# Kernel optimization log

Hardware: AMD Instinct MI355X
Metric: run time of the kernel (lower is better)

Reference implementation:

```python
import jax, jax.numpy as jnp
import numpy as np

TOKENS_PER_SCALE = [1, 4, 16, 64, 256]  # CLS + 2x2,4x4,8x8,16x16 patch scales = 341
TOTAL = sum(TOKENS_PER_SCALE)
NUM_HEADS = 12


def build_scale_causal_mask():
    # 0 where allowed, -inf where blocked. CLS row (scale 0) attends everywhere;
    # tokens in scale i may attend to scales j <= i (and always to CLS).
    cum = np.cumsum([0] + TOKENS_PER_SCALE)
    m = np.zeros((TOTAL, TOTAL), dtype=np.float32)
    for i in range(1, len(TOKENS_PER_SCALE)):
        for j in range(len(TOKENS_PER_SCALE)):
            if j > i:
                m[cum[i]:cum[i + 1], cum[j]:cum[j + 1]] = -np.inf
    return jnp.asarray(m)


def setup_inputs() -> dict:
    key = jax.random.key(0)
    k1, k2, k3, k4, k5 = jax.random.split(key, 5)
    B, N, D = 64, TOTAL, 768
    x = jax.random.normal(k1, (B, N, D), dtype=jnp.float32)
    qkv_w = jax.random.normal(k2, (3 * D, D), dtype=jnp.float32) * 0.02
    qkv_b = jax.random.normal(k3, (3 * D,), dtype=jnp.float32) * 0.02
    proj_w = jax.random.normal(k4, (D, D), dtype=jnp.float32) * 0.02
    proj_b = jax.random.normal(k5, (D,), dtype=jnp.float32) * 0.02
    return {"x": x, "qkv_w": qkv_w, "qkv_b": qkv_b, "proj_w": proj_w, "proj_b": proj_b}


def reference(x, qkv_w, qkv_b, proj_w, proj_b):
    B, N, D = x.shape
    H = NUM_HEADS
    hd = D // H
    scale = hd ** -0.5
    mask = build_scale_causal_mask()  # [N, N]

    qkv = jnp.einsum('bnd,ed->bne', x, qkv_w) + qkv_b  # [B, N, 3D]
    qkv = qkv.reshape(B, N, 3, H, hd)
    q = jnp.transpose(qkv[:, :, 0], (0, 2, 1, 3))  # [B, H, N, hd]
    k = jnp.transpose(qkv[:, :, 1], (0, 2, 1, 3))
    v = jnp.transpose(qkv[:, :, 2], (0, 2, 1, 3))

    attn = jnp.einsum('bhqd,bhkd->bhqk', q, k) * scale + mask  # [B, H, N, N]
    attn = jax.nn.softmax(attn, axis=-1)
    out = jnp.einsum('bhqk,bhkd->bhqd', attn, v)  # [B, H, N, hd]
    out = jnp.transpose(out, (0, 2, 1, 3)).reshape(B, N, D)
    out = jnp.einsum('bnd,ed->bne', out, proj_w) + proj_b
    return out
```

## Files before the change

kernel.cpp:

```cpp
#include <hip/hip_runtime.h>
#include <hip/hip_bf16.h>

typedef float  f32x4  __attribute__((ext_vector_type(4)));
typedef __bf16 bf16x4 __attribute__((ext_vector_type(4)));
typedef __bf16 bf16x8 __attribute__((ext_vector_type(8)));

#define B_SZ  64
#define NTOK  341
#define DM    768
#define NH    12
#define HD    64
#define MTOT  (B_SZ*NTOK)
#define MP    21888
#define EQKV  2304

#define EXP2F(x) __builtin_amdgcn_exp2f(x)

__device__ __forceinline__ void gload_lds16(const __bf16* g, void* l) {
    __builtin_amdgcn_global_load_lds(
        (const __attribute__((address_space(1))) void*)g,
        (__attribute__((address_space(3))) void*)l, 16, 0, 0);
}

__global__ void cvt_kernel(const float* __restrict__ in, __bf16* __restrict__ out, int n4) {
    int i = blockIdx.x * blockDim.x + threadIdx.x;
    const int stride = gridDim.x * blockDim.x;
    for (; i < n4; i += stride) {
        const float4 f = ((const float4*)in)[i];
        bf16x4 v;
        v[0] = (__bf16)f.x; v[1] = (__bf16)f.y; v[2] = (__bf16)f.z; v[3] = (__bf16)f.w;
        ((bf16x4*)out)[i] = v;
    }
}

template <int EPI, int EN, int NT>
__global__ __launch_bounds__(256) void gemm128(
    const __bf16* __restrict__ A, const __bf16* __restrict__ Bw,
    const float* __restrict__ bias,
    __bf16* __restrict__ obf, float* __restrict__ of32)
{
    __shared__ __bf16 As[2][128 * 64];
    __shared__ __bf16 Bs[2][128 * 64];

    const int tid  = threadIdx.x;
    const int lane = tid & 63;
    const int w    = tid >> 6;
    const int wm   = w >> 1, wn = w & 1;
    const int qi   = lane & 15;
    const int g    = lane >> 4;

    const int nwg = gridDim.x;
    const int bid = blockIdx.x;
    const int qq = nwg >> 3, rr = nwg & 7;
    const int xcd = bid & 7, idx = bid >> 3;
    const int wg = (xcd < rr ? xcd * (qq + 1) : rr * (qq + 1) + (xcd - rr) * qq) + idx;
    const int mtile = wg / NT;
    const int ntile = wg % NT;
    const long a_row0 = (long)mtile * 128;
    const long n0     = (long)ntile * 128;

    const int slot = lane & 7;
    const __bf16* aP[4];
    const __bf16* bP[4];
#pragma unroll
    for (int it = 0; it < 4; ++it) {
        const int lrow = it * 32 + w * 8 + (lane >> 3);
        const int scol = (slot ^ (lrow & 7)) * 8;
        aP[it] = A + (a_row0 + lrow) * DM + scol;
        const int gcol = (lrow & 64) | ((lrow & 15) << 2) | ((lrow >> 4) & 3);
        bP[it] = Bw + (n0 + gcol) * DM + scol;
    }

    const f32x4 fzero = {0.f, 0.f, 0.f, 0.f};
    f32x4 acc[4][4];
#pragma unroll
    for (int i = 0; i < 4; ++i)
#pragma unroll
        for (int j = 0; j < 4; ++j) acc[i][j] = fzero;

#define STAGE(P, K0) do { \
    _Pragma("unroll") for (int it = 0; it < 4; ++it) { \
        gload_lds16(aP[it] + (K0), (char*)(&As[P][0]) + it * 4096 + w * 1024); \
        gload_lds16(bP[it] + (K0), (char*)(&Bs[P][0]) + it * 4096 + w * 1024); \
    } } while (0)

    STAGE(0, 0);
    __syncthreads();

    int cur = 0;
    for (int k0 = 0; k0 < DM; k0 += 64) {
        if (k0 + 64 < DM) STAGE(cur ^ 1, k0 + 64);

        const __bf16* pA = &As[cur][0];
        const __bf16* pB = &Bs[cur][0];
        bf16x8 af[4][2], bfr[4][2];
#pragma unroll
        for (int i = 0; i < 4; ++i) {
            const int fr = wm * 64 + i * 16 + qi;
#pragma unroll
            for (int ks = 0; ks < 2; ++ks)
                af[i][ks] = *(const bf16x8*)(pA + fr * 64 + (((ks << 2) + g) ^ (fr & 7)) * 8);
        }
#pragma unroll
        for (int j = 0; j < 4; ++j) {
            const int frb = wn * 64 + j * 16 + qi;
#pragma unroll
            for (int ks = 0; ks < 2; ++ks)
                bfr[j][ks] = *(const bf16x8*)(pB + frb * 64 + (((ks << 2) + g) ^ (frb & 7)) * 8);
        }
#pragma unroll
        for (int ks = 0; ks < 2; ++ks)
#pragma unroll
            for (int j = 0; j < 4; ++j)
#pragma unroll
                for (int i = 0; i < 4; ++i)
                    acc[i][j] = __builtin_amdgcn_mfma_f32_16x16x32_bf16(
                        af[i][ks], bfr[j][ks], acc[i][j], 0, 0, 0);

        __syncthreads();
        cur ^= 1;
    }
#undef STAGE

    const long ge0 = n0 + wn * 64 + qi * 4;
    const float4 b4 = *(const float4*)(bias + ge0);
    const float mul = (EPI == 0 && (n0 + wn * 64) < DM) ? 0.125f * 1.44269504f : 1.f;
#pragma unroll
    for (int i = 0; i < 4; ++i) {
#pragma unroll
        for (int r = 0; r < 4; ++r) {
            const long m = a_row0 + wm * 64 + i * 16 + g * 4 + r;
            if (m < MTOT) {
                if (EPI == 0) {
                    bf16x4 pv;
                    pv[0] = (__bf16)((acc[i][0][r] + b4.x) * mul);
                    pv[1] = (__bf16)((acc[i][1][r] + b4.y) * mul);
                    pv[2] = (__bf16)((acc[i][2][r] + b4.z) * mul);
                    pv[3] = (__bf16)((acc[i][3][r] + b4.w) * mul);
                    *(bf16x4*)(obf + m * EN + ge0) = pv;
                } else {
                    float4 o;
                    o.x = acc[i][0][r] + b4.x;
                    o.y = acc[i][1][r] + b4.y;
                    o.z = acc[i][2][r] + b4.z;
                    o.w = acc[i][3][r] + b4.w;
                    *(float4*)(of32 + m * EN + ge0) = o;
                }
            }
        }
    }
}

template <int NJ>
__device__ __forceinline__ void attn_group(
    const __bf16* __restrict__ qkv, const char* vL, __bf16* __restrict__ ao,
    long rowb, int h, int q0, int qi, int g)
{
    int qrow = q0 + qi; if (qrow > NTOK - 1) qrow = NTOK - 1;
    const __bf16* qsrc = qkv + (rowb + qrow) * EQKV + h * HD + g * 8;
    const bf16x8 qf0 = *(const bf16x8*)(qsrc);
    const bf16x8 qf1 = *(const bf16x8*)(qsrc + 32);

    const int qg = q0 + qi;
    int limit;
    if (qg == 0)       limit = NTOK;
    else if (qg < 5)   limit = 5;
    else if (qg < 21)  limit = 21;
    else if (qg < 85)  limit = 85;
    else               limit = NTOK;

    const f32x4 fzero = {0.f, 0.f, 0.f, 0.f};
    f32x4 oacc[4] = {fzero, fzero, fzero, fzero};
    float sum = 0.f;

    const __bf16* kbase = qkv + rowb * EQKV + DM + h * HD + g * 8;
    const int xd = (qi & 7) ^ ((qi >> 3) & 7);

#pragma unroll 2
    for (int j = 0; j < NJ; ++j) {
        const int kr0 = 32 * j + qi;
        int kr1 = kr0 + 16; if (kr1 > NTOK - 1) kr1 = NTOK - 1;
        const __bf16* k0p = kbase + (long)kr0 * EQKV;
        const __bf16* k1p = kbase + (long)kr1 * EQKV;
        const bf16x8 k00 = *(const bf16x8*)(k0p);
        const bf16x8 k01 = *(const bf16x8*)(k0p + 32);
        const bf16x8 k10 = *(const bf16x8*)(k1p);
        const bf16x8 k11 = *(const bf16x8*)(k1p + 32);

        f32x4 s0 = __builtin_amdgcn_mfma_f32_16x16x32_bf16(k00, qf0, fzero, 0, 0, 0);
        s0 = __builtin_amdgcn_mfma_f32_16x16x32_bf16(k01, qf1, s0, 0, 0, 0);
        f32x4 s1 = __builtin_amdgcn_mfma_f32_16x16x32_bf16(k10, qf0, fzero, 0, 0, 0);
        s1 = __builtin_amdgcn_mfma_f32_16x16x32_bf16(k11, qf1, s1, 0, 0, 0);

        bf16x8 pf;
#pragma unroll
        for (int r = 0; r < 4; ++r) {
            const int k0i = 32 * j + g * 4 + r;
            const float p0 = (k0i < limit) ? EXP2F(s0[r]) : 0.f;
            sum += p0; pf[r] = (__bf16)p0;
            const int k1i = k0i + 16;
            const float p1 = (k1i < limit) ? EXP2F(s1[r]) : 0.f;
            sum += p1; pf[4 + r] = (__bf16)p1;
        }

#pragma unroll
        for (int db = 0; db < 4; ++db) {
            const int d  = db * 16 + qi;
            const int sp = (4 * j + g) ^ xd ^ ((2 * db) & 7);
            const bf16x8 vf = *(const bf16x8*)(vL + d * 768 + sp * 16);
            oacc[db] = __builtin_amdgcn_mfma_f32_16x16x32_bf16(vf, pf, oacc[db], 0, 0, 0);
        }
    }

    sum += __shfl_xor(sum, 16);
    sum += __shfl_xor(sum, 32);
    const float rinv = 1.f / sum;

    if (qg < NTOK) {
        const long orow = (rowb + qg) * DM + h * HD;
#pragma unroll
        for (int db = 0; db < 4; ++db) {
            bf16x4 pv;
#pragma unroll
            for (int r = 0; r < 4; ++r) pv[r] = (__bf16)(oacc[db][r] * rinv);
            *(bf16x4*)(ao + orow + db * 16 + g * 4) = pv;
        }
    }
}

__global__ __launch_bounds__(512) void attn_kernel(
    const __bf16* __restrict__ qkv, __bf16* __restrict__ ao)
{
    const int h = blockIdx.x;
    const int b = blockIdx.y;
    const long rowb = (long)b * NTOK;

    __shared__ char vL[64 * 768];

    const int tid  = threadIdx.x;
    const int lane = tid & 63;
    const int w    = tid >> 6;

#pragma unroll
    for (int it = 0; it < 6; ++it) {
        const int c = it * 512 + tid;
        if (c < 2816) {
            const int n  = c >> 3;
            const int dc = (c & 7) << 3;
            bf16x8 e;
            if (n < NTOK) e = *(const bf16x8*)(qkv + (rowb + n) * EQKV + 1536 + h * HD + dc);
            else { e[0]=e[1]=e[2]=e[3]=e[4]=e[5]=e[6]=e[7] = (__bf16)0.f; }
            const int s   = ((n >> 5) << 2) | ((n >> 2) & 3);
            const int off = (((n >> 4) & 1) << 3) | ((n & 3) << 1);
            const int x   = c & 7;
#pragma unroll
            for (int i = 0; i < 8; ++i) {
                const int sp = s ^ i ^ x;
                *(__bf16*)(vL + (dc + i) * 768 + sp * 16 + off) = e[i];
            }
        }
    }
    __syncthreads();

    const int g  = lane >> 4;
    const int qi = lane & 15;

    for (int gi = w; gi < 22; gi += 8) {
        const int q0 = gi * 16;
        if (gi >= 1 && gi <= 4)
            attn_group<3>(qkv, vL, ao, rowb, h, q0, qi, g);
        else
            attn_group<11>(qkv, vL, ao, rowb, h, q0, qi, g);
    }
}

extern "C" void kernel_launch(void* const* d_in, const int* in_sizes, int n_in,
                              void* d_out, int out_size, void* d_ws, size_t ws_size,
                              hipStream_t stream) {
    const float* x      = (const float*)d_in[0];
    const float* qkv_w  = (const float*)d_in[1];
    const float* qkv_b  = (const float*)d_in[2];
    const float* proj_w = (const float*)d_in[3];
    const float* proj_b = (const float*)d_in[4];
    float* out = (float*)d_out;

    char* ws = (char*)d_ws;
    constexpr size_t XB_BYTES  = (size_t)MP * DM * 2;
    constexpr size_t WQ_OFF    = XB_BYTES;
    constexpr size_t WP_OFF    = WQ_OFF + (size_t)EQKV * DM * 2;
    constexpr size_t QKV_OFF   = WP_OFF + (size_t)DM * DM * 2;

    __bf16* xb  = (__bf16*)(ws);
    __bf16* wq  = (__bf16*)(ws + WQ_OFF);
    __bf16* wp  = (__bf16*)(ws + WP_OFF);
    __bf16* qkv = (__bf16*)(ws + QKV_OFF);

    cvt_kernel<<<2048, 256, 0, stream>>>(x,      xb, MTOT * DM / 4);
    cvt_kernel<<<1728, 256, 0, stream>>>(qkv_w,  wq, EQKV * DM / 4);
    cvt_kernel<<<576,  256, 0, stream>>>(proj_w, wp, DM * DM / 4);

    gemm128<0, EQKV, 18><<<171 * 18, 256, 0, stream>>>(xb, wq, qkv_b, qkv, nullptr);
    attn_kernel<<<dim3(NH, B_SZ), 512, 0, stream>>>(qkv, xb);
    gemm128<1, DM, 6><<<171 * 6, 256, 0, stream>>>(xb, wp, proj_b, nullptr, out);
}
```

Measured before the change: 267.4 us.

## Process three query groups per wave to share K loads and V fragments

The attention kernel's per-wave loop over query groups is replaced by one pass in which each wave holds three 16-row query tiles at once. Each K fragment loaded from global memory and each V fragment read from LDS now feeds MFMAs for all three tiles, which cuts redundant loads and gives the scheduler more independent MFMA work. In exchange, the short three-iteration path for the early scales is dropped, so every tile runs all 11 key blocks. Two waves also compute out-of-range padding tiles whose results are thrown away, and accumulator register use triples.

```diff
diff --git a/kernel.cpp b/kernel.cpp
--- a/kernel.cpp
+++ b/kernel.cpp
@@ -151,83 +151,6 @@
     }
 }
 
-template <int NJ>
-__device__ __forceinline__ void attn_group(
-    const __bf16* __restrict__ qkv, const char* vL, __bf16* __restrict__ ao,
-    long rowb, int h, int q0, int qi, int g)
-{
-    int qrow = q0 + qi; if (qrow > NTOK - 1) qrow = NTOK - 1;
-    const __bf16* qsrc = qkv + (rowb + qrow) * EQKV + h * HD + g * 8;
-    const bf16x8 qf0 = *(const bf16x8*)(qsrc);
-    const bf16x8 qf1 = *(const bf16x8*)(qsrc + 32);
-
-    const int qg = q0 + qi;
-    int limit;
-    if (qg == 0)       limit = NTOK;
-    else if (qg < 5)   limit = 5;
-    else if (qg < 21)  limit = 21;
-    else if (qg < 85)  limit = 85;
-    else               limit = NTOK;
-
-    const f32x4 fzero = {0.f, 0.f, 0.f, 0.f};
-    f32x4 oacc[4] = {fzero, fzero, fzero, fzero};
-    float sum = 0.f;
-
-    const __bf16* kbase = qkv + rowb * EQKV + DM + h * HD + g * 8;
-    const int xd = (qi & 7) ^ ((qi >> 3) & 7);
-
-#pragma unroll 2
-    for (int j = 0; j < NJ; ++j) {
-        const int kr0 = 32 * j + qi;
-        int kr1 = kr0 + 16; if (kr1 > NTOK - 1) kr1 = NTOK - 1;
-        const __bf16* k0p = kbase + (long)kr0 * EQKV;
-        const __bf16* k1p = kbase + (long)kr1 * EQKV;
-        const bf16x8 k00 = *(const bf16x8*)(k0p);
-        const bf16x8 k01 = *(const bf16x8*)(k0p + 32);
-        const bf16x8 k10 = *(const bf16x8*)(k1p);
-        const bf16x8 k11 = *(const bf16x8*)(k1p + 32);
-
-        f32x4 s0 = __builtin_amdgcn_mfma_f32_16x16x32_bf16(k00, qf0, fzero, 0, 0, 0);
-        s0 = __builtin_amdgcn_mfma_f32_16x16x32_bf16(k01, qf1, s0, 0, 0, 0);
-        f32x4 s1 = __builtin_amdgcn_mfma_f32_16x16x32_bf16(k10, qf0, fzero, 0, 0, 0);
-        s1 = __builtin_amdgcn_mfma_f32_16x16x32_bf16(k11, qf1, s1, 0, 0, 0);
-
-        bf16x8 pf;
-#pragma unroll
-        for (int r = 0; r < 4; ++r) {
-            const int k0i = 32 * j + g * 4 + r;
-            const float p0 = (k0i < limit) ? EXP2F(s0[r]) : 0.f;
-            sum += p0; pf[r] = (__bf16)p0;
-            const int k1i = k0i + 16;
-            const float p1 = (k1i < limit) ? EXP2F(s1[r]) : 0.f;
-            sum += p1; pf[4 + r] = (__bf16)p1;
-        }
-
-#pragma unroll
-        for (int db = 0; db < 4; ++db) {
-            const int d  = db * 16 + qi;
-            const int sp = (4 * j + g) ^ xd ^ ((2 * db) & 7);
-            const bf16x8 vf = *(const bf16x8*)(vL + d * 768 + sp * 16);
-            oacc[db] = __builtin_amdgcn_mfma_f32_16x16x32_bf16(vf, pf, oacc[db], 0, 0, 0);
-        }
-    }
-
-    sum += __shfl_xor(sum, 16);
-    sum += __shfl_xor(sum, 32);
-    const float rinv = 1.f / sum;
-
-    if (qg < NTOK) {
-        const long orow = (rowb + qg) * DM + h * HD;
-#pragma unroll
-        for (int db = 0; db < 4; ++db) {
-            bf16x4 pv;
-#pragma unroll
-            for (int r = 0; r < 4; ++r) pv[r] = (__bf16)(oacc[db][r] * rinv);
-            *(bf16x4*)(ao + orow + db * 16 + g * 4) = pv;
-        }
-    }
-}
-
 __global__ __launch_bounds__(512) void attn_kernel(
     const __bf16* __restrict__ qkv, __bf16* __restrict__ ao)
 {
@@ -265,12 +188,87 @@
     const int g  = lane >> 4;
     const int qi = lane & 15;
 
-    for (int gi = w; gi < 22; gi += 8) {
-        const int q0 = gi * 16;
-        if (gi >= 1 && gi <= 4)
-            attn_group<3>(qkv, vL, ao, rowb, h, q0, qi, g);
-        else
-            attn_group<11>(qkv, vL, ao, rowb, h, q0, qi, g);
+    bf16x8 qf0[3], qf1[3];
+    int   qg[3], limit[3];
+#pragma unroll
+    for (int s = 0; s < 3; ++s) {
+        const int gi = w + 8 * s;
+        const int q  = gi * 16 + qi;
+        qg[s] = q;
+        const int qrow = (q > NTOK - 1) ? (NTOK - 1) : q;
+        const __bf16* qsrc = qkv + (rowb + qrow) * EQKV + h * HD + g * 8;
+        qf0[s] = *(const bf16x8*)(qsrc);
+        qf1[s] = *(const bf16x8*)(qsrc + 32);
+        limit[s] = (q == 0) ? NTOK : (q < 5 ? 5 : (q < 21 ? 21 : (q < 85 ? 85 : NTOK)));
+    }
+
+    const f32x4 fzero = {0.f, 0.f, 0.f, 0.f};
+    f32x4 oacc[3][4];
+    float sum[3] = {0.f, 0.f, 0.f};
+#pragma unroll
+    for (int s = 0; s < 3; ++s)
+#pragma unroll
+        for (int db = 0; db < 4; ++db) oacc[s][db] = fzero;
+
+    const __bf16* kbase = qkv + rowb * EQKV + DM + h * HD + g * 8;
+    const int xd = (qi & 7) ^ ((qi >> 3) & 7);
+
+    for (int j = 0; j < 11; ++j) {
+        const int kr0 = 32 * j + qi;
+        int kr1 = kr0 + 16; if (kr1 > NTOK - 1) kr1 = NTOK - 1;
+        const __bf16* k0p = kbase + (long)kr0 * EQKV;
+        const __bf16* k1p = kbase + (long)kr1 * EQKV;
+        const bf16x8 k00 = *(const bf16x8*)(k0p);
+        const bf16x8 k01 = *(const bf16x8*)(k0p + 32);
+        const bf16x8 k10 = *(const bf16x8*)(k1p);
+        const bf16x8 k11 = *(const bf16x8*)(k1p + 32);
+
+        bf16x8 pf[3];
+#pragma unroll
+        for (int s = 0; s < 3; ++s) {
+            f32x4 s0 = __builtin_amdgcn_mfma_f32_16x16x32_bf16(k00, qf0[s], fzero, 0, 0, 0);
+            s0 = __builtin_amdgcn_mfma_f32_16x16x32_bf16(k01, qf1[s], s0, 0, 0, 0);
+            f32x4 s1 = __builtin_amdgcn_mfma_f32_16x16x32_bf16(k10, qf0[s], fzero, 0, 0, 0);
+            s1 = __builtin_amdgcn_mfma_f32_16x16x32_bf16(k11, qf1[s], s1, 0, 0, 0);
+#pragma unroll
+            for (int r = 0; r < 4; ++r) {
+                const int k0i = 32 * j + g * 4 + r;
+                const float p0 = (k0i < limit[s]) ? EXP2F(s0[r]) : 0.f;
+                sum[s] += p0; pf[s][r] = (__bf16)p0;
+                const int k1i = k0i + 16;
+                const float p1 = (k1i < limit[s]) ? EXP2F(s1[r]) : 0.f;
+                sum[s] += p1; pf[s][4 + r] = (__bf16)p1;
+            }
+        }
+
+#pragma unroll
+        for (int db = 0; db < 4; ++db) {
+            const int d  = db * 16 + qi;
+            const int sp = (4 * j + g) ^ xd ^ ((2 * db) & 7);
+            const bf16x8 vf = *(const bf16x8*)(vL + d * 768 + sp * 16);
+#pragma unroll
+            for (int s = 0; s < 3; ++s)
+                oacc[s][db] = __builtin_amdgcn_mfma_f32_16x16x32_bf16(
+                    vf, pf[s], oacc[s][db], 0, 0, 0);
+        }
+    }
+
+#pragma unroll
+    for (int s = 0; s < 3; ++s) {
+        float t = sum[s];
+        t += __shfl_xor(t, 16);
+        t += __shfl_xor(t, 32);
+        const float rinv = 1.f / t;
+        if (qg[s] < NTOK) {
+            const long orow = (rowb + qg[s]) * DM + h * HD;
+#pragma unroll
+            for (int db = 0; db < 4; ++db) {
+                bf16x4 pv;
+#pragma unroll
+                for (int r = 0; r < 4; ++r) pv[r] = (__bf16)(oacc[s][db][r] * rinv);
+                *(bf16x4*)(ao + orow + db * 16 + g * 4) = pv;
+            }
+        }
     }
 }
 
```

Result: faster. 239.8 us (-10.3%).
